# Performance work log

Measured on AMD Instinct MI355X. Metric: run time of the kernel, lower is better.

Reference implementation:

```python
import jax, jax.numpy as jnp
import numpy as np

B, S, H, D = 2, 4096, 16, 128  # batch, seq, heads, head_dim
HID = H * D                    # 2048 hidden size
C = 128                        # chunk size for the chunked recurrent scan
EPS = 1e-6


def setup_inputs() -> dict:
    key = jax.random.key(0)
    ks = jax.random.split(key, 9)
    sc = 0.02  # initializer_range
    w = lambda k: jax.random.normal(k, (HID, HID), jnp.float32) * sc
    return {
        "x": jax.random.normal(ks[0], (B, S, HID), jnp.float32),
        "Wq": w(ks[1]), "bq": jnp.zeros((HID,), jnp.float32),
        "Wk": w(ks[2]), "bk": jnp.zeros((HID,), jnp.float32),
        "Wv": w(ks[3]), "bv": jnp.zeros((HID,), jnp.float32),
        "Wo": w(ks[4]), "bo": jnp.zeros((HID,), jnp.float32),
    }


def reference(x, Wq, bq, Wk, bk, Wv, bv, Wo, bo):
    Bx, Sx, hid = x.shape
    NC = Sx // C  # number of chunks

    q = (x @ Wq + bq).reshape(Bx, Sx, H, D)
    k = (x @ Wk + bk).reshape(Bx, Sx, H, D)
    v = (x @ Wv + bv).reshape(Bx, Sx, H, D)

    # positive feature map for linear attention
    qf = jax.nn.elu(q) + 1.0
    kf = jax.nn.elu(k) + 1.0

    # chunk: [B, NC, C, H, D]
    qf = qf.reshape(Bx, NC, C, H, D)
    kf = kf.reshape(Bx, NC, C, H, D)
    vc = v.reshape(Bx, NC, C, H, D)

    # inter-chunk recurrent state: exclusive cumulative sums of per-chunk KV outer
    kv = jnp.einsum('bnchd,bnche->bnhde', kf, vc)      # per-chunk KV state
    kv_ex = jnp.cumsum(kv, axis=1) - kv                # exclusive prefix state
    ksum = kf.sum(axis=2)                              # [B,NC,H,D]
    ksum_ex = jnp.cumsum(ksum, axis=1) - ksum          # exclusive normalizer state

    inter = jnp.einsum('bnchd,bnhde->bnche', qf, kv_ex)
    z_inter = jnp.einsum('bnchd,bnhd->bnch', qf, ksum_ex)

    # intra-chunk causal attention (masked matmul)
    A = jnp.einsum('bnchd,bnkhd->bnhck', qf, kf)       # [B,NC,H,C,C]
    causal = jnp.tril(jnp.ones((C, C), dtype=bool))
    A = jnp.where(causal[None, None, None], A, 0.0)
    intra = jnp.einsum('bnhck,bnkhe->bnche', A, vc)
    z_intra = jnp.swapaxes(A.sum(-1), 2, 3)            # [B,NC,C,H]

    out = (inter + intra) / (z_inter + z_intra + EPS)[..., None]
    out = out.reshape(Bx, Sx, hid)
    return out @ Wo + bo
```

## Files before the change

### kernel.cpp

```cpp
#include <hip/hip_runtime.h>

typedef unsigned short u16;
typedef unsigned int u32;
typedef unsigned long long u64;
typedef __attribute__((ext_vector_type(8))) short short8;
typedef __attribute__((ext_vector_type(4))) float f32x4;
typedef __attribute__((ext_vector_type(4))) int int4v;

constexpr int Bsz = 2, Ssz = 4096, Hn = 16, Dh = 128, HID = 2048;
constexpr int Cch = 128, NCh = 32;
constexpr float EPSf = 1e-6f;

#define MFMA16 __builtin_amdgcn_mfma_f32_16x16x32_bf16
#define VMCNT4 asm volatile("s_waitcnt vmcnt(4)" ::: "memory")
#define VMCNT0 asm volatile("s_waitcnt vmcnt(0)" ::: "memory")

__device__ __forceinline__ float b2f(u16 u) {
  unsigned int i = ((unsigned int)u) << 16;
  return __builtin_bit_cast(float, i);
}
__device__ __forceinline__ u16 f2b(float f) {
  unsigned int i = __builtin_bit_cast(unsigned int, f);
  i += 0x7fffu + ((i >> 16) & 1u);
  return (u16)(i >> 16);
}

__device__ __forceinline__ void gload_lds16(const u16* g, u16* l) {
  __builtin_amdgcn_global_load_lds(
      (const __attribute__((address_space(1))) u32*)g,
      (__attribute__((address_space(3))) u32*)l, 16, 0, 0);
}

__global__ __launch_bounds__(256) void cvt_bf16(const float* __restrict__ x,
                                                u16* __restrict__ xb)
{
  const size_t n8 = (size_t)Bsz * Ssz * HID / 8;
  for (size_t i = (size_t)blockIdx.x * 256 + threadIdx.x; i < n8;
       i += (size_t)gridDim.x * 256) {
    const f32x4 a = *(const f32x4*)&x[i * 8];
    const f32x4 b = *(const f32x4*)&x[i * 8 + 4];
    u16 tmp[8];
#pragma unroll
    for (int u = 0; u < 4; ++u) { tmp[u] = f2b(a[u]); tmp[u + 4] = f2b(b[u]); }
    *(int4v*)&xb[i * 8] = *(const int4v*)tmp;
  }
}

__global__ __launch_bounds__(256) void transpose4(
    const float* __restrict__ A0, const float* __restrict__ A1,
    const float* __restrict__ A2, const float* __restrict__ A3,
    u16* __restrict__ T0, u16* __restrict__ T1,
    u16* __restrict__ T2, u16* __restrict__ T3)
{
  constexpr int N = HID, LDT = 72;
  const int z = blockIdx.z;
  const float* __restrict__ A = (z == 0) ? A0 : (z == 1) ? A1 : (z == 2) ? A2 : A3;
  u16* __restrict__ T = (z == 0) ? T0 : (z == 1) ? T1 : (z == 2) ? T2 : T3;
  __shared__ u16 lds[64 * LDT];
  const int t = threadIdx.x;
  const int i = t >> 3, j = (t & 7) * 8;
  const int r0 = blockIdx.y * 64, c0 = blockIdx.x * 64;
#pragma unroll
  for (int half = 0; half < 2; ++half) {
    const int r = i + half * 32;
    const f32x4 a = *(const f32x4*)&A[(size_t)(r0 + r) * N + c0 + j];
    const f32x4 b = *(const f32x4*)&A[(size_t)(r0 + r) * N + c0 + j + 4];
    u16 tmp[8];
#pragma unroll
    for (int u = 0; u < 4; ++u) { tmp[u] = f2b(a[u]); tmp[u + 4] = f2b(b[u]); }
    *(int4v*)&lds[r * LDT + j] = *(const int4v*)tmp;
  }
  __syncthreads();
#pragma unroll
  for (int half = 0; half < 2; ++half) {
    const int c = i + half * 32;
    u16 tmp[8];
#pragma unroll
    for (int u = 0; u < 8; ++u) tmp[u] = lds[(j + u) * LDT + c];
    *(int4v*)&T[(size_t)(c0 + c) * N + r0 + j] = *(const int4v*)tmp;
  }
}

template <int OUTF32>
__global__ __launch_bounds__(512) void gemm8p(
    const u16* __restrict__ A,
    const u16* __restrict__ W0T, const u16* __restrict__ W1T, const u16* __restrict__ W2T,
    const float* __restrict__ bb0, const float* __restrict__ bb1, const float* __restrict__ bb2,
    void* __restrict__ o0, void* __restrict__ o1, void* __restrict__ o2,
    int elu_mask)
{
  constexpr int K = HID, N = HID;
  constexpr int NT = K / 64;
  extern __shared__ u16 lds[];

  const int z = blockIdx.z;
  const u16* __restrict__ WT    = (z == 0) ? W0T : (z == 1) ? W1T : W2T;
  const float* __restrict__ bias = (z == 0) ? bb0 : (z == 1) ? bb1 : bb2;
  void* __restrict__ outv = (z == 0) ? o0 : (z == 1) ? o1 : o2;
  const bool elu = (elu_mask >> z) & 1;

  const int lid = blockIdx.x + 8 * blockIdx.y;
  const int wlid = (lid & 7) * 32 + (lid >> 3);
  const int n0 = (wlid >> 5) * 256;
  const int m0 = (wlid & 31) * 256;

  const int t = threadIdx.x, lane = t & 63, w = t >> 6;
  const int wm = w >> 2, wn = w & 3;
  const int l15 = lane & 15, lg = lane >> 4;
  const int sl2 = (l15 >> 1) & 3;

  const int strow = lane >> 2;
  const int stslot = (lane & 3) ^ ((lane >> 3) & 3);
  const u16* gA = A  + (size_t)(m0 + w * 16 + strow) * K + stslot * 8;
  const u16* gB = WT + (size_t)(n0 + w * 16 + strow) * K + stslot * 8;

  auto stage = [&](int buf, int mat, int h, int kt) {
    const u16* g = (mat ? gB : gA) + (size_t)kt * 64 + h * 32;
    u16* l = &lds[buf * 32768 + mat * 16384 + h * 8192 + w * 512];
    gload_lds16(g, l);
    gload_lds16(g + (size_t)128 * K, l + 4096);
  };
  auto rdA = [&](int buf, int i, int kk) -> short8 {
    return *(const short8*)&lds[buf * 32768 + kk * 8192 +
                                (wm * 128 + i * 16 + l15) * 32 + ((lg ^ sl2) << 3)];
  };
  auto rdB = [&](int buf, int j, int kk) -> short8 {
    return *(const short8*)&lds[buf * 32768 + 16384 + kk * 8192 +
                                (wn * 64 + j * 16 + l15) * 32 + ((lg ^ sl2) << 3)];
  };

  f32x4 acc[8][4] = {};
  short8 aF[8], b0, b1;

  stage(0, 0, 0, 0);
  stage(0, 1, 0, 0);
  stage(0, 0, 1, 0);
  stage(0, 1, 1, 0);
  VMCNT4;
  __builtin_amdgcn_s_barrier();

  for (int W = 0; W < NT; ++W) {
    const int buf = W & 1, sb = buf ^ 1, kn = W + 1;
    const bool ds = kn < NT;
#pragma unroll
    for (int i = 0; i < 8; ++i) aF[i] = rdA(buf, i, 0);
    b0 = rdB(buf, 0, 0); b1 = rdB(buf, 1, 0);
    if (ds) stage(sb, 0, 0, kn);
    __builtin_amdgcn_s_barrier();
    __builtin_amdgcn_s_setprio(1);
#pragma unroll
    for (int i = 0; i < 8; ++i) {
      acc[i][0] = MFMA16(aF[i], b0, acc[i][0], 0, 0, 0);
      acc[i][1] = MFMA16(aF[i], b1, acc[i][1], 0, 0, 0);
    }
    __builtin_amdgcn_s_setprio(0);
    __builtin_amdgcn_s_barrier();
    b0 = rdB(buf, 2, 0); b1 = rdB(buf, 3, 0);
    if (ds) stage(sb, 1, 0, kn);
    __builtin_amdgcn_s_barrier();
    __builtin_amdgcn_s_setprio(1);
#pragma unroll
    for (int i = 0; i < 8; ++i) {
      acc[i][2] = MFMA16(aF[i], b0, acc[i][2], 0, 0, 0);
      acc[i][3] = MFMA16(aF[i], b1, acc[i][3], 0, 0, 0);
    }
    __builtin_amdgcn_s_setprio(0);
    if (ds) { VMCNT4; } else { VMCNT0; }
    __builtin_amdgcn_s_barrier();
#pragma unroll
    for (int i = 0; i < 8; ++i) aF[i] = rdA(buf, i, 1);
    b0 = rdB(buf, 0, 1); b1 = rdB(buf, 1, 1);
    if (ds) stage(sb, 0, 1, kn);
    __builtin_amdgcn_s_barrier();
    __builtin_amdgcn_s_setprio(1);
#pragma unroll
    for (int i = 0; i < 8; ++i) {
      acc[i][0] = MFMA16(aF[i], b0, acc[i][0], 0, 0, 0);
      acc[i][1] = MFMA16(aF[i], b1, acc[i][1], 0, 0, 0);
    }
    __builtin_amdgcn_s_setprio(0);
    __builtin_amdgcn_s_barrier();
    b0 = rdB(buf, 2, 1); b1 = rdB(buf, 3, 1);
    if (ds) stage(sb, 1, 1, kn);
    __builtin_amdgcn_s_barrier();
    __builtin_amdgcn_s_setprio(1);
#pragma unroll
    for (int i = 0; i < 8; ++i) {
      acc[i][2] = MFMA16(aF[i], b0, acc[i][2], 0, 0, 0);
      acc[i][3] = MFMA16(aF[i], b1, acc[i][3], 0, 0, 0);
    }
    __builtin_amdgcn_s_setprio(0);
    if (ds) { VMCNT4; __builtin_amdgcn_s_barrier(); }
  }

#pragma unroll
  for (int j = 0; j < 4; ++j) {
    const int col = n0 + wn * 64 + j * 16 + l15;
    const float bv = bias[col];
#pragma unroll
    for (int i = 0; i < 8; ++i) {
      const int row0 = m0 + wm * 128 + i * 16 + lg * 4;
#pragma unroll
      for (int r = 0; r < 4; ++r) {
        float v = acc[i][j][r] + bv;
        if (elu) v = (v > 0.0f) ? (v + 1.0f) : __expf(v);
        if (OUTF32) ((float*)outv)[(size_t)(row0 + r) * N + col] = v;
        else        ((u16*)outv)[(size_t)(row0 + r) * N + col] = f2b(v);
      }
    }
  }
}

__global__ __launch_bounds__(256) void pass1_kv(
    const u16* __restrict__ KF, const u16* __restrict__ V,
    u16* __restrict__ KVT, float* __restrict__ KSUM)
{
  constexpr int LD = 136;
  __shared__ u16 lk[128 * LD];
  __shared__ u16 lv[128 * LD];
  const int bnh = blockIdx.x;
  const int h = bnh % Hn, n = (bnh / Hn) % NCh, b = bnh / (Hn * NCh);
  const size_t rowbase = (size_t)(b * Ssz + n * Cch) * HID + h * Dh;
  const int t = threadIdx.x, lane = t & 63, w = t >> 6;
  const int wr = (w >> 1) * 64, wc = (w & 1) * 64;
  const int l15 = lane & 15, lg = lane >> 4;
  const int sr = t >> 4, sc = (t & 15) * 8;

#pragma unroll
  for (int rep = 0; rep < 8; ++rep) {
    const int r = rep * 16 + sr;
    *(int4v*)&lk[r * LD + sc] = *(const int4v*)&KF[rowbase + (size_t)r * HID + sc];
    *(int4v*)&lv[r * LD + sc] = *(const int4v*)&V[rowbase + (size_t)r * HID + sc];
  }
  __syncthreads();

  if (t < 128) {
    float s = 0.0f;
    for (int c = 0; c < 128; ++c) s += b2f(lk[c * LD + t]);
    KSUM[(size_t)bnh * Dh + t] = s;
  }

  f32x4 acc[4][4] = {};
#pragma unroll
  for (int kk = 0; kk < 4; ++kk) {
    const int cb = kk * 32 + lg * 8;
    short8 aF[4], bF[4];
#pragma unroll
    for (int i = 0; i < 4; ++i) {
      const int e = wr + i * 16 + l15;
      short8 a;
#pragma unroll
      for (int u = 0; u < 8; ++u) a[u] = (short)lv[(cb + u) * LD + e];
      aF[i] = a;
    }
#pragma unroll
    for (int j = 0; j < 4; ++j) {
      const int d = wc + j * 16 + l15;
      short8 bb;
#pragma unroll
      for (int u = 0; u < 8; ++u) bb[u] = (short)lk[(cb + u) * LD + d];
      bF[j] = bb;
    }
#pragma unroll
    for (int i = 0; i < 4; ++i)
#pragma unroll
      for (int j = 0; j < 4; ++j)
        acc[i][j] = MFMA16(aF[i], bF[j], acc[i][j], 0, 0, 0);
  }

  u16* __restrict__ outp = KVT + (size_t)bnh * (Dh * Dh);
#pragma unroll
  for (int i = 0; i < 4; ++i) {
    const int e0 = wr + i * 16 + lg * 4;
#pragma unroll
    for (int j = 0; j < 4; ++j) {
      const int d = wc + j * 16 + l15;
#pragma unroll
      for (int r = 0; r < 4; ++r)
        outp[(size_t)(e0 + r) * Dh + d] = f2b(acc[i][j][r]);
    }
  }
}

__global__ __launch_bounds__(256) void cumsum_kv(u16* __restrict__ KVT) {
  const int tid = blockIdx.x * 256 + threadIdx.x;
  const int ed = tid & (Dh * Dh - 1);
  const int bh = tid >> 14;
  const int h = bh % Hn, b = bh / Hn;
  const size_t base = ((size_t)(b * NCh * Hn) + h) * (Dh * Dh) + ed;
  const size_t stride = (size_t)Hn * Dh * Dh;
  float s = 0.0f;
  for (int n = 0; n < NCh; ++n) {
    const size_t idx = base + (size_t)n * stride;
    const float v = b2f(KVT[idx]);
    KVT[idx] = f2b(s);
    s += v;
  }
}

__global__ __launch_bounds__(256) void cumsum_ks(float* __restrict__ KS) {
  const int tid = blockIdx.x * 256 + threadIdx.x;
  const int d = tid & (Dh - 1);
  const int bh = tid >> 7;
  const int h = bh % Hn, b = bh / Hn;
  const size_t base = ((size_t)(b * NCh * Hn) + h) * Dh + d;
  const size_t stride = (size_t)Hn * Dh;
  float s = 0.0f;
  for (int n = 0; n < NCh; ++n) {
    const size_t idx = base + (size_t)n * stride;
    const float v = KS[idx];
    KS[idx] = s;
    s += v;
  }
}

__global__ __launch_bounds__(256) void pass2_attn(
    const u16* __restrict__ QF, const u16* __restrict__ KF, const u16* __restrict__ V,
    const u16* __restrict__ KVT, const float* __restrict__ KSE,
    u16* __restrict__ Y)
{
  constexpr int LD = 136;
  __shared__ u16 smem[4 * 128 * LD];
  __shared__ float zbuf[128];
  u16* sQ  = smem;
  u16* sK  = smem + 128 * LD;
  u16* sA  = smem + 2 * 128 * LD;
  u16* sKV = smem + 3 * 128 * LD;

  const int bnh = blockIdx.x;
  const int h = bnh % Hn, n = (bnh / Hn) % NCh, b = bnh / (Hn * NCh);
  const size_t rowbase = (size_t)(b * Ssz + n * Cch) * HID + h * Dh;
  const int t = threadIdx.x, lane = t & 63, w = t >> 6;
  const int wr = (w >> 1) * 64, wc = (w & 1) * 64;
  const int l15 = lane & 15, lg = lane >> 4;
  const int sr = t >> 4, sc = (t & 15) * 8;

  const u16* __restrict__ kvsrc = KVT + (size_t)bnh * (Dh * Dh);
#pragma unroll
  for (int rep = 0; rep < 8; ++rep) {
    const int r = rep * 16 + sr;
    *(int4v*)&sQ[r * LD + sc]  = *(const int4v*)&QF[rowbase + (size_t)r * HID + sc];
    *(int4v*)&sK[r * LD + sc]  = *(const int4v*)&KF[rowbase + (size_t)r * HID + sc];
    *(int4v*)&sKV[r * LD + sc] = *(const int4v*)&kvsrc[r * Dh + sc];
  }
  __syncthreads();

  f32x4 acc[4][4] = {};
#pragma unroll
  for (int kk = 0; kk < 4; ++kk) {
    const int krd = kk * 32 + lg * 8;
    short8 aF[4], bF[4];
#pragma unroll
    for (int i = 0; i < 4; ++i)
      aF[i] = *(const short8*)&sQ[(wr + i * 16 + l15) * LD + krd];
#pragma unroll
    for (int j = 0; j < 4; ++j)
      bF[j] = *(const short8*)&sK[(wc + j * 16 + l15) * LD + krd];
#pragma unroll
    for (int i = 0; i < 4; ++i)
#pragma unroll
      for (int j = 0; j < 4; ++j)
        acc[i][j] = MFMA16(aF[i], bF[j], acc[i][j], 0, 0, 0);
  }
#pragma unroll
  for (int i = 0; i < 4; ++i) {
    const int c0 = wr + i * 16 + lg * 4;
#pragma unroll
    for (int j = 0; j < 4; ++j) {
      const int ck = wc + j * 16 + l15;
#pragma unroll
      for (int r = 0; r < 4; ++r) {
        const int c = c0 + r;
        sA[c * LD + ck] = f2b((ck <= c) ? acc[i][j][r] : 0.0f);
      }
    }
  }
  __syncthreads();

  if (t < 128) {
    const float* kse = KSE + (size_t)bnh * Dh;
    float zz = EPSf;
    for (int d2 = 0; d2 < 128; ++d2) zz += b2f(sQ[t * LD + d2]) * kse[d2];
    for (int ck = 0; ck < 128; ++ck) zz += b2f(sA[t * LD + ck]);
    zbuf[t] = zz;
  }
#pragma unroll
  for (int rep = 0; rep < 8; ++rep) {
    const int r = rep * 16 + sr;
    *(int4v*)&sK[r * LD + sc] = *(const int4v*)&V[rowbase + (size_t)r * HID + sc];
  }
  __syncthreads();

  f32x4 o[4][4] = {};
#pragma unroll
  for (int kk = 0; kk < 4; ++kk) {
    const int krd = kk * 32 + lg * 8;
    short8 aF[4], bF[4];
#pragma unroll
    for (int i = 0; i < 4; ++i)
      aF[i] = *(const short8*)&sA[(wr + i * 16 + l15) * LD + krd];
#pragma unroll
    for (int j = 0; j < 4; ++j) {
      const int e = wc + j * 16 + l15;
      short8 bb;
#pragma unroll
      for (int u = 0; u < 8; ++u) bb[u] = (short)sK[(krd + u) * LD + e];
      bF[j] = bb;
    }
#pragma unroll
    for (int i = 0; i < 4; ++i)
#pragma unroll
      for (int j = 0; j < 4; ++j)
        o[i][j] = MFMA16(aF[i], bF[j], o[i][j], 0, 0, 0);
  }
#pragma unroll
  for (int kk = 0; kk < 4; ++kk) {
    const int krd = kk * 32 + lg * 8;
    short8 aF[4], bF[4];
#pragma unroll
    for (int i = 0; i < 4; ++i)
      aF[i] = *(const short8*)&sQ[(wr + i * 16 + l15) * LD + krd];
#pragma unroll
    for (int j = 0; j < 4; ++j)
      bF[j] = *(const short8*)&sKV[(wc + j * 16 + l15) * LD + krd];
#pragma unroll
    for (int i = 0; i < 4; ++i)
#pragma unroll
      for (int j = 0; j < 4; ++j)
        o[i][j] = MFMA16(aF[i], bF[j], o[i][j], 0, 0, 0);
  }

#pragma unroll
  for (int i = 0; i < 4; ++i) {
    const int c0 = wr + i * 16 + lg * 4;
#pragma unroll
    for (int j = 0; j < 4; ++j) {
      const int e = wc + j * 16 + l15;
#pragma unroll
      for (int r = 0; r < 4; ++r) {
        const int c = c0 + r;
        Y[rowbase + (size_t)c * HID + e] = f2b(o[i][j][r] / zbuf[c]);
      }
    }
  }
}

extern "C" void kernel_launch(void* const* d_in, const int* in_sizes, int n_in,
                              void* d_out, int out_size, void* d_ws, size_t ws_size,
                              hipStream_t stream)
{
  const float* x  = (const float*)d_in[0];
  const float* Wq = (const float*)d_in[1];
  const float* bq = (const float*)d_in[2];
  const float* Wk = (const float*)d_in[3];
  const float* bk = (const float*)d_in[4];
  const float* Wv = (const float*)d_in[5];
  const float* bv = (const float*)d_in[6];
  const float* Wo = (const float*)d_in[7];
  const float* bo = (const float*)d_in[8];
  float* out = (float*)d_out;

  char* p = (char*)d_ws;
  auto take = [&](size_t bytes) { char* q = p; p += (bytes + 255) & ~(size_t)255; return q; };
  u16* WqT = (u16*)take((size_t)HID * HID * 2);
  u16* WkT = (u16*)take((size_t)HID * HID * 2);
  u16* WvT = (u16*)take((size_t)HID * HID * 2);
  u16* WoT = (u16*)take((size_t)HID * HID * 2);
  u16* QF  = (u16*)take((size_t)Bsz * Ssz * HID * 2);
  u16* KFb = (u16*)take((size_t)Bsz * Ssz * HID * 2);
  u16* Vb  = (u16*)take((size_t)Bsz * Ssz * HID * 2);
  char* region = take((size_t)Bsz * Ssz * HID * 2);
  u16* xb  = (u16*)region;
  u16* KVT = (u16*)region;
  float* KS = (float*)take((size_t)Bsz * NCh * Hn * Dh * 4);
  u16* Yb = QF;

  (void)hipFuncSetAttribute((const void*)gemm8p<0>,
                            hipFuncAttributeMaxDynamicSharedMemorySize, 131072);
  (void)hipFuncSetAttribute((const void*)gemm8p<1>,
                            hipFuncAttributeMaxDynamicSharedMemorySize, 131072);

  dim3 blk(256, 1, 1);
  cvt_bf16<<<dim3(2048), blk, 0, stream>>>(x, xb);
  transpose4<<<dim3(HID / 64, HID / 64, 4), blk, 0, stream>>>(
      Wq, Wk, Wv, Wo, WqT, WkT, WvT, WoT);
  gemm8p<0><<<dim3(HID / 256, (Bsz * Ssz) / 256, 3), dim3(512), 131072, stream>>>(
      xb, WqT, WkT, WvT, bq, bk, bv, QF, KFb, Vb, 0x3);
  pass1_kv<<<dim3(Bsz * NCh * Hn), blk, 0, stream>>>(KFb, Vb, KVT, KS);
  cumsum_kv<<<dim3((Bsz * Hn * Dh * Dh) / 256), blk, 0, stream>>>(KVT);
  cumsum_ks<<<dim3((Bsz * Hn * Dh) / 256), blk, 0, stream>>>(KS);
  pass2_attn<<<dim3(Bsz * NCh * Hn), blk, 0, stream>>>(QF, KFb, Vb, KVT, KS, Yb);
  gemm8p<1><<<dim3(HID / 256, (Bsz * Ssz) / 256, 1), dim3(512), 131072, stream>>>(
      Yb, WoT, WoT, WoT, bo, bo, bo, out, out, out, 0);
}
```

Before: 425.8 us.

## Restructure GEMM main loop into two halves per k-tile with fewer barriers

Rewrites the bf16 MFMA GEMM inner loop so each k-tile is processed in two halves. Each half loads all eight A fragments and all four B fragments at once, issues the prefetch of A and B for the next buffer together, and runs all 32 MFMAs without an intermediate barrier. The loop is unrolled by two so buffer indices become compile-time constants, and the global pointers are advanced incrementally. The aim is to halve the barrier count and cut address arithmetic; in exchange more fragment registers are live and the load-to-MFMA interleaving is coarser.

Result: no change. 418.5 us (-1.7%).

```diff
diff --git a/kernel.cpp b/kernel.cpp
--- a/kernel.cpp
+++ b/kernel.cpp
@@ -82,7 +82,7 @@
 }
 
 template <int OUTF32>
-__global__ __launch_bounds__(512) void gemm8p(
+__global__ __launch_bounds__(512) void gemm2b(
     const u16* __restrict__ A,
     const u16* __restrict__ W0T, const u16* __restrict__ W1T, const u16* __restrict__ W2T,
     const float* __restrict__ bb0, const float* __restrict__ bb1, const float* __restrict__ bb2,
@@ -114,83 +114,59 @@
   const u16* gA = A  + (size_t)(m0 + w * 16 + strow) * K + stslot * 8;
   const u16* gB = WT + (size_t)(n0 + w * 16 + strow) * K + stslot * 8;
 
-  auto stage = [&](int buf, int mat, int h, int kt) {
-    const u16* g = (mat ? gB : gA) + (size_t)kt * 64 + h * 32;
-    u16* l = &lds[buf * 32768 + mat * 16384 + h * 8192 + w * 512];
-    gload_lds16(g, l);
-    gload_lds16(g + (size_t)128 * K, l + 4096);
-  };
-  auto rdA = [&](int buf, int i, int kk) -> short8 {
-    return *(const short8*)&lds[buf * 32768 + kk * 8192 +
-                                (wm * 128 + i * 16 + l15) * 32 + ((lg ^ sl2) << 3)];
-  };
-  auto rdB = [&](int buf, int j, int kk) -> short8 {
-    return *(const short8*)&lds[buf * 32768 + 16384 + kk * 8192 +
-                                (wn * 64 + j * 16 + l15) * 32 + ((lg ^ sl2) << 3)];
-  };
+  const int aRow = (wm * 128 + l15) * 32 + ((lg ^ sl2) << 3);
+  const int bRow = 16384 + (wn * 64 + l15) * 32 + ((lg ^ sl2) << 3);
+  u16* const lw = &lds[w * 512];
 
   f32x4 acc[8][4] = {};
-  short8 aF[8], b0, b1;
-
-  stage(0, 0, 0, 0);
-  stage(0, 1, 0, 0);
-  stage(0, 0, 1, 0);
-  stage(0, 1, 1, 0);
+  short8 aF[8], bF[4];
+
+#define STAGE(SB, KKC) do {                                                   \
+    gload_lds16(gA + (KKC) * 32,                 lw + (SB)*32768 + (KKC)*8192);          \
+    gload_lds16(gA + (KKC) * 32 + (size_t)128*K, lw + (SB)*32768 + (KKC)*8192 + 4096);   \
+    gload_lds16(gB + (KKC) * 32,                 lw + (SB)*32768 + 16384 + (KKC)*8192);  \
+    gload_lds16(gB + (KKC) * 32 + (size_t)128*K, lw + (SB)*32768 + 16384 + (KKC)*8192 + 4096); \
+  } while (0)
+
+#define HALF(BUF, KKC, PF) do {                                               \
+    _Pragma("unroll")                                                         \
+    for (int i = 0; i < 8; ++i)                                               \
+      aF[i] = *(const short8*)&lds[(BUF)*32768 + (KKC)*8192 + aRow + i*512];  \
+    _Pragma("unroll")                                                         \
+    for (int j = 0; j < 4; ++j)                                               \
+      bF[j] = *(const short8*)&lds[(BUF)*32768 + (KKC)*8192 + bRow + j*512];  \
+    if (PF) STAGE((BUF)^1, KKC);                                              \
+    __builtin_amdgcn_s_setprio(1);                                            \
+    _Pragma("unroll")                                                         \
+    for (int i = 0; i < 8; ++i) {                                             \
+      acc[i][0] = MFMA16(aF[i], bF[0], acc[i][0], 0, 0, 0);                   \
+      acc[i][1] = MFMA16(aF[i], bF[1], acc[i][1], 0, 0, 0);                   \
+      acc[i][2] = MFMA16(aF[i], bF[2], acc[i][2], 0, 0, 0);                   \
+      acc[i][3] = MFMA16(aF[i], bF[3], acc[i][3], 0, 0, 0);                   \
+    }                                                                         \
+    __builtin_amdgcn_s_setprio(0);                                            \
+  } while (0)
+
+  STAGE(0, 0);
+  STAGE(0, 1);
+  gA += 64; gB += 64;
   VMCNT4;
   __builtin_amdgcn_s_barrier();
 
-  for (int W = 0; W < NT; ++W) {
-    const int buf = W & 1, sb = buf ^ 1, kn = W + 1;
-    const bool ds = kn < NT;
-#pragma unroll
-    for (int i = 0; i < 8; ++i) aF[i] = rdA(buf, i, 0);
-    b0 = rdB(buf, 0, 0); b1 = rdB(buf, 1, 0);
-    if (ds) stage(sb, 0, 0, kn);
+  for (int W = 0; W < NT; W += 2) {
+    const bool p0 = (W + 1) < NT, p1 = (W + 2) < NT;
+    HALF(0, 0, p0);
+    if (p0) { VMCNT4; } else { VMCNT0; }
     __builtin_amdgcn_s_barrier();
-    __builtin_amdgcn_s_setprio(1);
-#pragma unroll
-    for (int i = 0; i < 8; ++i) {
-      acc[i][0] = MFMA16(aF[i], b0, acc[i][0], 0, 0, 0);
-      acc[i][1] = MFMA16(aF[i], b1, acc[i][1], 0, 0, 0);
-    }
-    __builtin_amdgcn_s_setprio(0);
-    __builtin_amdgcn_s_barrier();
-    b0 = rdB(buf, 2, 0); b1 = rdB(buf, 3, 0);
-    if (ds) stage(sb, 1, 0, kn);
-    __builtin_amdgcn_s_barrier();
-    __builtin_amdgcn_s_setprio(1);
-#pragma unroll
-    for (int i = 0; i < 8; ++i) {
-      acc[i][2] = MFMA16(aF[i], b0, acc[i][2], 0, 0, 0);
-      acc[i][3] = MFMA16(aF[i], b1, acc[i][3], 0, 0, 0);
-    }
-    __builtin_amdgcn_s_setprio(0);
-    if (ds) { VMCNT4; } else { VMCNT0; }
-    __builtin_amdgcn_s_barrier();
-#pragma unroll
-    for (int i = 0; i < 8; ++i) aF[i] = rdA(buf, i, 1);
-    b0 = rdB(buf, 0, 1); b1 = rdB(buf, 1, 1);
-    if (ds) stage(sb, 0, 1, kn);
-    __builtin_amdgcn_s_barrier();
-    __builtin_amdgcn_s_setprio(1);
-#pragma unroll
-    for (int i = 0; i < 8; ++i) {
-      acc[i][0] = MFMA16(aF[i], b0, acc[i][0], 0, 0, 0);
-      acc[i][1] = MFMA16(aF[i], b1, acc[i][1], 0, 0, 0);
-    }
-    __builtin_amdgcn_s_setprio(0);
-    __builtin_amdgcn_s_barrier();
-    b0 = rdB(buf, 2, 1); b1 = rdB(buf, 3, 1);
-    if (ds) stage(sb, 1, 1, kn);
-    __builtin_amdgcn_s_barrier();
-    __builtin_amdgcn_s_setprio(1);
-#pragma unroll
-    for (int i = 0; i < 8; ++i) {
-      acc[i][2] = MFMA16(aF[i], b0, acc[i][2], 0, 0, 0);
-      acc[i][3] = MFMA16(aF[i], b1, acc[i][3], 0, 0, 0);
-    }
-    __builtin_amdgcn_s_setprio(0);
-    if (ds) { VMCNT4; __builtin_amdgcn_s_barrier(); }
+    HALF(0, 1, p0);
+    if (p0) { gA += 64; gB += 64; VMCNT4; __builtin_amdgcn_s_barrier(); }
+    if (p0) {
+      HALF(1, 0, p1);
+      if (p1) { VMCNT4; } else { VMCNT0; }
+      __builtin_amdgcn_s_barrier();
+      HALF(1, 1, p1);
+      if (p1) { gA += 64; gB += 64; VMCNT4; __builtin_amdgcn_s_barrier(); }
+    }
   }
 
 #pragma unroll
@@ -209,6 +185,8 @@
       }
     }
   }
+#undef STAGE
+#undef HALF
 }
 
 __global__ __launch_bounds__(256) void pass1_kv(
@@ -475,21 +453,21 @@
   float* KS = (float*)take((size_t)Bsz * NCh * Hn * Dh * 4);
   u16* Yb = QF;
 
-  (void)hipFuncSetAttribute((const void*)gemm8p<0>,
+  (void)hipFuncSetAttribute((const void*)gemm2b<0>,
                             hipFuncAttributeMaxDynamicSharedMemorySize, 131072);
-  (void)hipFuncSetAttribute((const void*)gemm8p<1>,
+  (void)hipFuncSetAttribute((const void*)gemm2b<1>,
                             hipFuncAttributeMaxDynamicSharedMemorySize, 131072);
 
   dim3 blk(256, 1, 1);
   cvt_bf16<<<dim3(2048), blk, 0, stream>>>(x, xb);
   transpose4<<<dim3(HID / 64, HID / 64, 4), blk, 0, stream>>>(
       Wq, Wk, Wv, Wo, WqT, WkT, WvT, WoT);
-  gemm8p<0><<<dim3(HID / 256, (Bsz * Ssz) / 256, 3), dim3(512), 131072, stream>>>(
+  gemm2b<0><<<dim3(HID / 256, (Bsz * Ssz) / 256, 3), dim3(512), 131072, stream>>>(
       xb, WqT, WkT, WvT, bq, bk, bv, QF, KFb, Vb, 0x3);
   pass1_kv<<<dim3(Bsz * NCh * Hn), blk, 0, stream>>>(KFb, Vb, KVT, KS);
   cumsum_kv<<<dim3((Bsz * Hn * Dh * Dh) / 256), blk, 0, stream>>>(KVT);
   cumsum_ks<<<dim3((Bsz * Hn * Dh) / 256), blk, 0, stream>>>(KS);
   pass2_attn<<<dim3(Bsz * NCh * Hn), blk, 0, stream>>>(QF, KFb, Vb, KVT, KS, Yb);
-  gemm8p<1><<<dim3(HID / 256, (Bsz * Ssz) / 256, 1), dim3(512), 131072, stream>>>(
+  gemm2b<1><<<dim3(HID / 256, (Bsz * Ssz) / 256, 1), dim3(512), 131072, stream>>>(
       Yb, WoT, WoT, WoT, bo, bo, bo, out, out, out, 0);
 }
```
